# Kernel tuning notes

Measured on AMD Instinct MI355X. Metric: run time of the kernel, lower is better.

## Reference

```python
import jax, jax.numpy as jnp
import numpy as np

K = 256
TAU = 1.0


def setup_inputs() -> dict:
    key = jax.random.key(0)
    scores = jax.random.normal(key, (32, 2048), dtype=jnp.float32)
    return {"scores": scores}


def reference(scores) -> jnp.ndarray:
    # scores: [B, dim]
    bsize, dim = scores.shape
    s = scores[:, :, None]  # [B, dim, 1]
    # B_i = sum_j |s_i - s_j|  -> [B, dim, 1]
    A = jnp.abs(s - scores[:, None, :])  # [B, dim, dim]
    Bsum = jnp.sum(A, axis=-1, keepdims=True)  # [B, dim, 1]
    # scaling: (dim + 1 - 2*(i+1)) for i in 0..k-1
    scaling = (dim + 1 - 2 * (jnp.arange(K) + 1)).astype(scores.dtype)  # [k]
    C = s * scaling[None, None, :]  # [B, dim, k] (outer product)
    P_max = jnp.transpose(C - Bsum, (0, 2, 1))  # [B, k, dim]
    P_hat = jax.nn.softmax(P_max / TAU, axis=-1)
    return P_hat
```

## Files before the change

### kernel.cpp

```cpp
#include <hip/hip_runtime.h>
#include <math.h>

#define DIM 2048
#define NB 32
#define NK 256

__global__ __launch_bounds__(256) void bsum_kernel(const float* __restrict__ scores,
                                                   float* __restrict__ bsum) {
    __shared__ float4 srow[128];
    const int b  = blockIdx.z;
    const int j0 = blockIdx.y * 512;
    const int i0 = blockIdx.x * 1024;
    const float* row = scores + b * DIM;

    if (threadIdx.x < 128) srow[threadIdx.x] = ((const float4*)(row + j0))[threadIdx.x];
    __syncthreads();

    const float4 xi = ((const float4*)(row + i0))[threadIdx.x];
    float a0 = 0.f, a1 = 0.f, a2 = 0.f, a3 = 0.f;
    #pragma unroll 4
    for (int jj = 0; jj < 128; ++jj) {
        const float4 xj = srow[jj];
        a0 += (fabsf(xi.x - xj.x) + fabsf(xi.x - xj.y)) + (fabsf(xi.x - xj.z) + fabsf(xi.x - xj.w));
        a1 += (fabsf(xi.y - xj.x) + fabsf(xi.y - xj.y)) + (fabsf(xi.y - xj.z) + fabsf(xi.y - xj.w));
        a2 += (fabsf(xi.z - xj.x) + fabsf(xi.z - xj.y)) + (fabsf(xi.z - xj.z) + fabsf(xi.z - xj.w));
        a3 += (fabsf(xi.w - xj.x) + fabsf(xi.w - xj.y)) + (fabsf(xi.w - xj.z) + fabsf(xi.w - xj.w));
    }
    const int i = i0 + threadIdx.x * 4;
    float* dst = bsum + b * DIM + i;
    atomicAdd(dst + 0, a0);
    atomicAdd(dst + 1, a1);
    atomicAdd(dst + 2, a2);
    atomicAdd(dst + 3, a3);
}

__global__ __launch_bounds__(256) void softmax_kernel(const float* __restrict__ scores,
                                                      const float* __restrict__ bsum,
                                                      float* __restrict__ out) {
    const int k   = blockIdx.x;
    const int b   = blockIdx.y;
    const int tid = threadIdx.x;
    const float scale = (float)(DIM - 1 - 2 * k);

    const float4* s4  = (const float4*)(scores + b * DIM);
    const float4* bs4 = (const float4*)(bsum   + b * DIM);
    const float4 sA = s4[2 * tid],  sB = s4[2 * tid + 1];
    const float4 bA = bs4[2 * tid], bB = bs4[2 * tid + 1];

    float t[8];
    t[0] = sA.x * scale - bA.x;  t[1] = sA.y * scale - bA.y;
    t[2] = sA.z * scale - bA.z;  t[3] = sA.w * scale - bA.w;
    t[4] = sB.x * scale - bB.x;  t[5] = sB.y * scale - bB.y;
    t[6] = sB.z * scale - bB.z;  t[7] = sB.w * scale - bB.w;

    float m = t[0];
    #pragma unroll
    for (int q = 1; q < 8; ++q) m = fmaxf(m, t[q]);
    #pragma unroll
    for (int off = 32; off > 0; off >>= 1) m = fmaxf(m, __shfl_xor(m, off, 64));

    __shared__ float redm[4];
    __shared__ float reds[4];
    const int wid = tid >> 6;
    if ((tid & 63) == 0) redm[wid] = m;
    __syncthreads();
    m = fmaxf(fmaxf(redm[0], redm[1]), fmaxf(redm[2], redm[3]));

    float e[8];
    float s = 0.f;
    #pragma unroll
    for (int q = 0; q < 8; ++q) { e[q] = __expf(t[q] - m); s += e[q]; }
    #pragma unroll
    for (int off = 32; off > 0; off >>= 1) s += __shfl_xor(s, off, 64);
    if ((tid & 63) == 0) reds[wid] = s;
    __syncthreads();
    s = (reds[0] + reds[1]) + (reds[2] + reds[3]);

    const float inv = 1.f / s;
    float4* o4 = (float4*)(out + ((size_t)(b * NK + k)) * DIM);
    float4 o;
    o.x = e[0] * inv; o.y = e[1] * inv; o.z = e[2] * inv; o.w = e[3] * inv;
    o4[2 * tid] = o;
    o.x = e[4] * inv; o.y = e[5] * inv; o.z = e[6] * inv; o.w = e[7] * inv;
    o4[2 * tid + 1] = o;
}

extern "C" void kernel_launch(void* const* d_in, const int* in_sizes, int n_in,
                              void* d_out, int out_size, void* d_ws, size_t ws_size,
                              hipStream_t stream) {
    const float* scores = (const float*)d_in[0];
    float* out  = (float*)d_out;
    float* bsum = (float*)d_ws;

    hipMemsetAsync(bsum, 0, (size_t)NB * DIM * sizeof(float), stream);
    bsum_kernel<<<dim3(2, 4, NB), 256, 0, stream>>>(scores, bsum);
    softmax_kernel<<<dim3(NK, NB), 256, 0, stream>>>(scores, bsum, out);
}
```

Before: 96.92 us.

## Drop atomics/memset in bsum and use single-wave softmax blocks handling two rows

The bsum kernel now stages the whole row in shared memory and each thread computes the full sum for one element, writing it directly. That removes the memset and the atomic adds. The softmax kernel uses 64-thread single-wavefront blocks that each handle two k rows, reusing loaded scores and bsum. Wave shuffles replace the shared-memory reductions and barriers. The trade-off is more per-thread work in bsum (2048 iterations per thread) and higher register use in softmax.

Result: no change. 97.47 us (+0.6%).

```diff
diff --git a/kernel.cpp b/kernel.cpp
--- a/kernel.cpp
+++ b/kernel.cpp
@@ -4,85 +4,101 @@
 #define DIM 2048
 #define NB 32
 #define NK 256
+#define KPB 2
 
 __global__ __launch_bounds__(256) void bsum_kernel(const float* __restrict__ scores,
                                                    float* __restrict__ bsum) {
-    __shared__ float4 srow[128];
-    const int b  = blockIdx.z;
-    const int j0 = blockIdx.y * 512;
-    const int i0 = blockIdx.x * 1024;
+    __shared__ float4 srow[DIM / 4];
+    const int b = blockIdx.y;
+    const int t = threadIdx.x;
     const float* row = scores + b * DIM;
 
-    if (threadIdx.x < 128) srow[threadIdx.x] = ((const float4*)(row + j0))[threadIdx.x];
+    srow[t]       = ((const float4*)row)[t];
+    srow[t + 256] = ((const float4*)row)[t + 256];
     __syncthreads();
 
-    const float4 xi = ((const float4*)(row + i0))[threadIdx.x];
+    const int i = blockIdx.x * 256 + t;
+    const float xi = ((const float*)srow)[i];
+
     float a0 = 0.f, a1 = 0.f, a2 = 0.f, a3 = 0.f;
     #pragma unroll 4
-    for (int jj = 0; jj < 128; ++jj) {
+    for (int jj = 0; jj < DIM / 4; ++jj) {
         const float4 xj = srow[jj];
-        a0 += (fabsf(xi.x - xj.x) + fabsf(xi.x - xj.y)) + (fabsf(xi.x - xj.z) + fabsf(xi.x - xj.w));
-        a1 += (fabsf(xi.y - xj.x) + fabsf(xi.y - xj.y)) + (fabsf(xi.y - xj.z) + fabsf(xi.y - xj.w));
-        a2 += (fabsf(xi.z - xj.x) + fabsf(xi.z - xj.y)) + (fabsf(xi.z - xj.z) + fabsf(xi.z - xj.w));
-        a3 += (fabsf(xi.w - xj.x) + fabsf(xi.w - xj.y)) + (fabsf(xi.w - xj.z) + fabsf(xi.w - xj.w));
+        a0 += fabsf(xi - xj.x);
+        a1 += fabsf(xi - xj.y);
+        a2 += fabsf(xi - xj.z);
+        a3 += fabsf(xi - xj.w);
     }
-    const int i = i0 + threadIdx.x * 4;
-    float* dst = bsum + b * DIM + i;
-    atomicAdd(dst + 0, a0);
-    atomicAdd(dst + 1, a1);
-    atomicAdd(dst + 2, a2);
-    atomicAdd(dst + 3, a3);
+    bsum[b * DIM + i] = (a0 + a1) + (a2 + a3);
 }
 
-__global__ __launch_bounds__(256) void softmax_kernel(const float* __restrict__ scores,
-                                                      const float* __restrict__ bsum,
-                                                      float* __restrict__ out) {
-    const int k   = blockIdx.x;
-    const int b   = blockIdx.y;
-    const int tid = threadIdx.x;
-    const float scale = (float)(DIM - 1 - 2 * k);
+__global__ __launch_bounds__(64) void softmax_kernel(const float* __restrict__ scores,
+                                                     const float* __restrict__ bsum,
+                                                     float* __restrict__ out) {
+    const int b  = blockIdx.y;
+    const int k0 = blockIdx.x * KPB;
+    const int t  = threadIdx.x;
 
     const float4* s4  = (const float4*)(scores + b * DIM);
     const float4* bs4 = (const float4*)(bsum   + b * DIM);
-    const float4 sA = s4[2 * tid],  sB = s4[2 * tid + 1];
-    const float4 bA = bs4[2 * tid], bB = bs4[2 * tid + 1];
 
-    float t[8];
-    t[0] = sA.x * scale - bA.x;  t[1] = sA.y * scale - bA.y;
-    t[2] = sA.z * scale - bA.z;  t[3] = sA.w * scale - bA.w;
-    t[4] = sB.x * scale - bB.x;  t[5] = sB.y * scale - bB.y;
-    t[6] = sB.z * scale - bB.z;  t[7] = sB.w * scale - bB.w;
+    float4 sv[8], bv[8];
+    #pragma unroll
+    for (int q = 0; q < 8; ++q) {
+        sv[q] = s4[t + 64 * q];
+        bv[q] = bs4[t + 64 * q];
+    }
 
-    float m = t[0];
     #pragma unroll
-    for (int q = 1; q < 8; ++q) m = fmaxf(m, t[q]);
-    #pragma unroll
-    for (int off = 32; off > 0; off >>= 1) m = fmaxf(m, __shfl_xor(m, off, 64));
+    for (int kk = 0; kk < KPB; ++kk) {
+        const int k = k0 + kk;
+        const float scale = (float)(DIM - 1 - 2 * k);
 
-    __shared__ float redm[4];
-    __shared__ float reds[4];
-    const int wid = tid >> 6;
-    if ((tid & 63) == 0) redm[wid] = m;
-    __syncthreads();
-    m = fmaxf(fmaxf(redm[0], redm[1]), fmaxf(redm[2], redm[3]));
+        float e[32];
+        #pragma unroll
+        for (int q = 0; q < 8; ++q) {
+            e[4 * q + 0] = fmaf(sv[q].x, scale, -bv[q].x);
+            e[4 * q + 1] = fmaf(sv[q].y, scale, -bv[q].y);
+            e[4 * q + 2] = fmaf(sv[q].z, scale, -bv[q].z);
+            e[4 * q + 3] = fmaf(sv[q].w, scale, -bv[q].w);
+        }
 
-    float e[8];
-    float s = 0.f;
-    #pragma unroll
-    for (int q = 0; q < 8; ++q) { e[q] = __expf(t[q] - m); s += e[q]; }
-    #pragma unroll
-    for (int off = 32; off > 0; off >>= 1) s += __shfl_xor(s, off, 64);
-    if ((tid & 63) == 0) reds[wid] = s;
-    __syncthreads();
-    s = (reds[0] + reds[1]) + (reds[2] + reds[3]);
+        float m0 = e[0], m1 = e[1], m2 = e[2], m3 = e[3];
+        #pragma unroll
+        for (int j = 4; j < 32; j += 4) {
+            m0 = fmaxf(m0, e[j + 0]);
+            m1 = fmaxf(m1, e[j + 1]);
+            m2 = fmaxf(m2, e[j + 2]);
+            m3 = fmaxf(m3, e[j + 3]);
+        }
+        float m = fmaxf(fmaxf(m0, m1), fmaxf(m2, m3));
+        #pragma unroll
+        for (int off = 32; off > 0; off >>= 1) m = fmaxf(m, __shfl_xor(m, off, 64));
 
-    const float inv = 1.f / s;
-    float4* o4 = (float4*)(out + ((size_t)(b * NK + k)) * DIM);
-    float4 o;
-    o.x = e[0] * inv; o.y = e[1] * inv; o.z = e[2] * inv; o.w = e[3] * inv;
-    o4[2 * tid] = o;
-    o.x = e[4] * inv; o.y = e[5] * inv; o.z = e[6] * inv; o.w = e[7] * inv;
-    o4[2 * tid + 1] = o;
+        float s0 = 0.f, s1 = 0.f, s2 = 0.f, s3 = 0.f;
+        #pragma unroll
+        for (int j = 0; j < 32; j += 4) {
+            e[j + 0] = __expf(e[j + 0] - m); s0 += e[j + 0];
+            e[j + 1] = __expf(e[j + 1] - m); s1 += e[j + 1];
+            e[j + 2] = __expf(e[j + 2] - m); s2 += e[j + 2];
+            e[j + 3] = __expf(e[j + 3] - m); s3 += e[j + 3];
+        }
+        float s = (s0 + s1) + (s2 + s3);
+        #pragma unroll
+        for (int off = 32; off > 0; off >>= 1) s += __shfl_xor(s, off, 64);
+
+        const float inv = 1.f / s;
+        float4* o4 = (float4*)(out + ((size_t)(b * NK + k)) * DIM);
+        #pragma unroll
+        for (int q = 0; q < 8; ++q) {
+            float4 o;
+            o.x = e[4 * q + 0] * inv;
+            o.y = e[4 * q + 1] * inv;
+            o.z = e[4 * q + 2] * inv;
+            o.w = e[4 * q + 3] * inv;
+            o4[t + 64 * q] = o;
+        }
+    }
 }
 
 extern "C" void kernel_launch(void* const* d_in, const int* in_sizes, int n_in,
@@ -92,7 +108,6 @@
     float* out  = (float*)d_out;
     float* bsum = (float*)d_ws;
 
-    hipMemsetAsync(bsum, 0, (size_t)NB * DIM * sizeof(float), stream);
-    bsum_kernel<<<dim3(2, 4, NB), 256, 0, stream>>>(scores, bsum);
-    softmax_kernel<<<dim3(NK, NB), 256, 0, stream>>>(scores, bsum, out);
+    bsum_kernel<<<dim3(8, NB), 256, 0, stream>>>(scores, bsum);
+    softmax_kernel<<<dim3(NK / KPB, NB), 64, 0, stream>>>(scores, bsum, out);
 }
```
